# Performance work log

Measured on AMD Instinct MI355X. Metric: run time of the kernel, lower is better.

The kernel has to match this reference:

```python
import jax, jax.numpy as jnp
import numpy as np

N = 16384   # total nodes per drug-batch
E = 65536   # directed edges (avg degree 4)
B = 512     # graphs per batch
BN_EPS = 1e-5
SLOPE = 0.01  # LeakyReLU default


def _rn(k, shape, s=0.02):
    return jax.random.normal(k, shape, dtype=jnp.float32) * s


def setup_inputs():
    key = jax.random.key(0)
    ks = jax.random.split(key, 32)
    d = {}
    d['x1'] = jax.random.normal(ks[0], (N, 78), dtype=jnp.float32)
    d['edge_index1'] = jax.random.randint(ks[1], (2, E), 0, N)
    d['batch1'] = jnp.sort(jax.random.randint(ks[2], (N,), 0, B))
    d['x2'] = jax.random.normal(ks[3], (N, 78), dtype=jnp.float32)
    d['edge_index2'] = jax.random.randint(ks[4], (2, E), 0, N)
    d['batch2'] = jnp.sort(jax.random.randint(ks[5], (N,), 0, B))
    d['cell'] = jax.random.normal(ks[6], (B, 954), dtype=jnp.float32)
    # TransformerConv1: 78 -> 2 heads x 128 (concat 256)
    d['wq1'] = _rn(ks[7], (78, 256));  d['bq1'] = jnp.zeros((256,), jnp.float32)
    d['wk1'] = _rn(ks[8], (78, 256));  d['bk1'] = jnp.zeros((256,), jnp.float32)
    d['wv1'] = _rn(ks[9], (78, 256));  d['bv1'] = jnp.zeros((256,), jnp.float32)
    d['ws1'] = _rn(ks[10], (78, 256)); d['bs1'] = jnp.zeros((256,), jnp.float32)
    # TransformerConv2: 256 -> 2 heads x 512 (concat 1024)
    d['wq2'] = _rn(ks[11], (256, 1024)); d['bq2'] = jnp.zeros((1024,), jnp.float32)
    d['wk2'] = _rn(ks[12], (256, 1024)); d['bk2'] = jnp.zeros((1024,), jnp.float32)
    d['wv2'] = _rn(ks[13], (256, 1024)); d['bv2'] = jnp.zeros((1024,), jnp.float32)
    d['ws2'] = _rn(ks[14], (256, 1024)); d['bs2'] = jnp.zeros((1024,), jnp.float32)
    d['wg1'] = _rn(ks[15], (1024, 512)); d['bg1'] = jnp.zeros((512,), jnp.float32)
    d['wg2'] = _rn(ks[16], (512, 128));  d['bg2'] = jnp.zeros((128,), jnp.float32)
    d['wr1'] = _rn(ks[17], (954, 512));  d['br1'] = jnp.zeros((512,), jnp.float32)
    d['wr2'] = _rn(ks[18], (512, 256));  d['br2'] = jnp.zeros((256,), jnp.float32)
    d['wr3'] = _rn(ks[19], (256, 128));  d['br3'] = jnp.zeros((128,), jnp.float32)
    d['wf1'] = _rn(ks[20], (384, 512));  d['bf1'] = jnp.zeros((512,), jnp.float32)
    d['gbn1'] = jnp.ones((512,), jnp.float32); d['bbn1'] = jnp.zeros((512,), jnp.float32)
    d['wf2'] = _rn(ks[21], (512, 256));  d['bf2'] = jnp.zeros((256,), jnp.float32)
    d['gbn2'] = jnp.ones((256,), jnp.float32); d['bbn2'] = jnp.zeros((256,), jnp.float32)
    d['wf3'] = _rn(ks[22], (256, 1));    d['bf3'] = jnp.zeros((1,), jnp.float32)
    return d


def _lrelu(x):
    return jnp.where(x >= 0, x, SLOPE * x)


def _l2n(x):
    return x / jnp.maximum(jnp.linalg.norm(x, axis=1, keepdims=True), 1e-12)


def _tconv(x, ei, wq, bq, wk, bk, wv, bv, ws, bs, H, D):
    # PyG TransformerConv (concat=True, beta=False, root_weight=True)
    src, dst = ei[0], ei[1]
    n = x.shape[0]
    q = (x @ wq + bq).reshape(n, H, D)
    k = (x @ wk + bk).reshape(n, H, D)
    v = (x @ wv + bv).reshape(n, H, D)
    logits = jnp.einsum('ehd,ehd->eh', q[dst], k[src]) / jnp.sqrt(jnp.float32(D))  # [E,H]
    m = jax.ops.segment_max(logits, dst, num_segments=n)
    m = jnp.where(jnp.isfinite(m), m, 0.0)
    e = jnp.exp(logits - m[dst])
    z = jax.ops.segment_sum(e, dst, num_segments=n)
    alpha = e / (z[dst] + 1e-16)
    agg = jax.ops.segment_sum(alpha[:, :, None] * v[src], dst, num_segments=n)  # [N,H,D]
    return agg.reshape(n, H * D) + x @ ws + bs


def reference(x1, edge_index1, batch1, x2, edge_index2, batch2, cell,
              wq1, bq1, wk1, bk1, wv1, bv1, ws1, bs1,
              wq2, bq2, wk2, bk2, wv2, bv2, ws2, bs2,
              wg1, bg1, wg2, bg2, wr1, br1, wr2, br2, wr3, br3,
              wf1, bf1, gbn1, bbn1, wf2, bf2, gbn2, bbn2, wf3, bf3):
    def branch(x, ei, bt):
        h = _lrelu(_tconv(x, ei, wq1, bq1, wk1, bk1, wv1, bv1, ws1, bs1, 2, 128))
        h = _lrelu(_tconv(h, ei, wq2, bq2, wk2, bk2, wv2, bv2, ws2, bs2, 2, 512))
        g = jax.ops.segment_max(h, bt, num_segments=B)  # global max pool per graph
        g = jnp.where(jnp.isfinite(g), g, 0.0)
        g = _lrelu(g @ wg1 + bg1)
        g = g @ wg2 + bg2  # dropout = identity in eval
        return _l2n(g)

    x1g = branch(x1, edge_index1, batch1)
    x2g = branch(x2, edge_index2, batch2)

    c = _l2n(cell)
    c = _lrelu(c @ wr1 + br1)
    c = _lrelu(c @ wr2 + br2)
    c = c @ wr3 + br3

    xc = _l2n(jnp.concatenate([x1g, x2g, c], axis=1))  # [B, 384]
    bn = 1.0 / jnp.sqrt(1.0 + BN_EPS)  # eval BN with running mean 0, var 1
    h = _lrelu((xc @ wf1 + bf1) * bn * gbn1 + bbn1)
    h = _lrelu((h @ wf2 + bf2) * bn * gbn2 + bbn2)
    return jax.nn.sigmoid((h @ wf3 + bf3)[:, 0])
```

## Files before the change

kernel.cpp:

```cpp
#include <hip/hip_runtime.h>
#include <hip/hip_bf16.h>
#include <hip/hip_fp8.h>
#include <math.h>
#include <stdint.h>

typedef __hip_bfloat16 bf16;

#define NN 16384
#define EE 65536
#define BB 512

typedef __attribute__((ext_vector_type(8))) short short8;
typedef __attribute__((ext_vector_type(2))) short short2v;
typedef __attribute__((ext_vector_type(4))) float floatx4;
typedef __attribute__((ext_vector_type(2))) float floatx2;
typedef __attribute__((ext_vector_type(2))) unsigned int uint2v;

#define GKEY_NEGINF 0x007FFFFFu

__device__ __forceinline__ float lrelu_f(float x){ return x >= 0.f ? x : 0.01f*x; }

__device__ __forceinline__ float b2f(short s){
    unsigned int u = ((unsigned int)(unsigned short)s) << 16;
    float f; __builtin_memcpy(&f, &u, 4); return f;
}
__device__ __forceinline__ short f2b(float f){
    bf16 b = (bf16)f;
    short s; __builtin_memcpy(&s, &b, 2); return s;
}
__device__ __forceinline__ unsigned int fkey(float f){
    unsigned int u; __builtin_memcpy(&u, &f, 4);
    return (u & 0x80000000u) ? ~u : (u | 0x80000000u);
}
__device__ __forceinline__ float fdec(unsigned int k){
    if (k == GKEY_NEGINF) return 0.f;
    unsigned int u = (k & 0x80000000u) ? (k ^ 0x80000000u) : ~k;
    float f; __builtin_memcpy(&f, &u, 4); return f;
}

__device__ __forceinline__ void gl2lds16(const void* g, void* l){
    __builtin_amdgcn_global_load_lds(
        (__attribute__((address_space(1))) unsigned int*)(uintptr_t)g,
        (__attribute__((address_space(3))) unsigned int*)(uintptr_t)l, 16, 0, 0);
}

template<int KSC>
__global__ __launch_bounds__(256)
void mfma_gemm(const bf16* __restrict__ A, int lda,
               const bf16* __restrict__ Bp,
               const float* __restrict__ bias,
               bf16* __restrict__ C, int ldc,
               unsigned char* __restrict__ C2, int ldc2, int nsplit)
{
    __shared__ __align__(16) char smem[20480];
    bf16* As0 = (bf16*)smem;
    bf16* As1 = (bf16*)(smem + 8192);
    bf16* epi = (bf16*)smem;
    const int tid  = threadIdx.x;
    const int wave = tid >> 6;
    const int lane = tid & 63;
    const int wm = (wave & 1) * 64;
    const int wn = (wave >> 1) * 64;
    const int m0 = blockIdx.x * 128;
    const int n0 = blockIdx.y * 128;
    const bool isf8 = (n0 >= nsplit);
    const int ntile0 = (n0 + wn) >> 4;

    const int srow = lane >> 2;
    const int scol = (((lane & 3) ^ ((srow >> 1) & 3))) * 8;
    const int arow = lane & 15;
    const int aq   = (((lane >> 4) ^ ((arow >> 1) & 3))) * 8;

    floatx4 acc[4][4];
    #pragma unroll
    for (int i=0;i<4;i++)
        #pragma unroll
        for (int j=0;j<4;j++) acc[i][j] = (floatx4){0.f,0.f,0.f,0.f};

    auto stageA = [&](int t, bf16* buf){
        const int k0 = t*32;
        #pragma unroll
        for (int i = 0; i < 2; i++) {
            const int chunk = wave*2 + i;
            const int r = chunk*16 + srow;
            gl2lds16(A + (size_t)(m0 + r)*lda + k0 + scol, buf + chunk*512);
        }
    };
    auto loadB = [&](short8* dst, int ks){
        #pragma unroll
        for (int j=0;j<4;j++)
            dst[j] = *(const short8*)(Bp + ((size_t)((ntile0 + j)*KSC + ks))*512 + lane*8);
    };

    short8 bcur[4], bnxt[4];
    loadB(bcur, 0);
    stageA(0, As0);

    #pragma unroll
    for (int t = 0; t < KSC; t++){
        bf16* cur = (t & 1) ? As1 : As0;
        bf16* nxt = (t & 1) ? As0 : As1;
        if (t + 1 < KSC){
            stageA(t+1, nxt);
            loadB(bnxt, t+1);
            asm volatile("s_waitcnt vmcnt(6)" ::: "memory");
        } else {
            asm volatile("s_waitcnt vmcnt(0)" ::: "memory");
        }
        __builtin_amdgcn_s_barrier();
        __builtin_amdgcn_sched_barrier(0);
        short8 af[4];
        #pragma unroll
        for (int i=0;i<4;i++) af[i] = *(const short8*)(cur + (wm + i*16 + arow)*32 + aq);
        #pragma unroll
        for (int i=0;i<4;i++)
            #pragma unroll
            for (int j=0;j<4;j++)
                acc[i][j] = __builtin_amdgcn_mfma_f32_16x16x32_bf16(af[i], bcur[j], acc[i][j], 0,0,0);
        __builtin_amdgcn_sched_barrier(0);
        __builtin_amdgcn_s_barrier();
        if (t + 1 < KSC){
            #pragma unroll
            for (int j=0;j<4;j++) bcur[j] = bnxt[j];
        }
    }

    const int crow = (lane >> 4) * 4;
    const int ccol = lane & 15;
    const int erow = lane >> 2;
    const int ecol = (lane & 3) * 8;
    bf16* ep = epi + wave * (64*40);
    #pragma unroll
    for (int j2 = 0; j2 < 2; j2++){
        if (j2) __syncthreads();
        #pragma unroll
        for (int jj = 0; jj < 2; jj++){
            const int j = j2*2 + jj;
            const float bsv = bias[n0 + wn + j*16 + ccol];
            #pragma unroll
            for (int i = 0; i < 4; i++)
                #pragma unroll
                for (int r = 0; r < 4; r++)
                    ep[(i*16 + crow + r)*40 + jj*16 + ccol] = (bf16)(acc[i][j][r] + bsv);
        }
        __syncthreads();
        #pragma unroll
        for (int q = 0; q < 4; q++){
            const int rr = q*16 + erow;
            short8 vv = *(const short8*)(ep + rr*40 + ecol);
            if (!isf8){
                *(short8*)(C + (size_t)(m0 + wm + rr)*ldc + n0 + wn + j2*32 + ecol) = vv;
            } else {
                int d0 = 0, d1 = 0;
                d0 = __builtin_amdgcn_cvt_pk_fp8_f32(b2f(vv[0]), b2f(vv[1]), d0, false);
                d0 = __builtin_amdgcn_cvt_pk_fp8_f32(b2f(vv[2]), b2f(vv[3]), d0, true);
                d1 = __builtin_amdgcn_cvt_pk_fp8_f32(b2f(vv[4]), b2f(vv[5]), d1, false);
                d1 = __builtin_amdgcn_cvt_pk_fp8_f32(b2f(vv[6]), b2f(vv[7]), d1, true);
                uint2v ob; ob[0] = (unsigned int)d0; ob[1] = (unsigned int)d1;
                *(uint2v*)(C2 + (size_t)(m0 + wm + rr)*ldc2 + (n0 - nsplit) + wn + j2*32 + ecol) = ob;
            }
        }
    }
}

#define OG1 0
#define OG2 524288
#define OR1 589824
#define OR2 1081344
#define OR3 1212416
#define OF1 1245184
#define OF2 1441792
#define TAILW_TOTAL 1572864

#define P_W1T 98304
#define P_B1C (P_W1T + 1024)
#define P_W2T (P_B1C + 1048576)
#define P_B2C (P_W2T + 4096)
#define P_WTP (P_B2C + TAILW_TOTAL)
#define P_XA  (P_WTP + 2*NN*96)
#define P_GK  (P_XA + 2*BB*1024)
__global__ void prep_mega_kernel(
    const float* __restrict__ wq1, const float* __restrict__ wk1,
    const float* __restrict__ wv1, const float* __restrict__ ws1,
    const float* __restrict__ bq1, const float* __restrict__ bk1,
    const float* __restrict__ bv1, const float* __restrict__ bs1,
    const float* __restrict__ wq2, const float* __restrict__ wk2,
    const float* __restrict__ wv2, const float* __restrict__ ws2,
    const float* __restrict__ bq2, const float* __restrict__ bk2,
    const float* __restrict__ bv2, const float* __restrict__ bs2v,
    const float* __restrict__ wg1, const float* __restrict__ wg2,
    const float* __restrict__ wr1, const float* __restrict__ wr2,
    const float* __restrict__ wr3, const float* __restrict__ wf1,
    const float* __restrict__ wf2,
    const float* __restrict__ x1,  const float* __restrict__ x2,
    bf16* __restrict__ W1t, float* __restrict__ b1c,
    bf16* __restrict__ W2t, float* __restrict__ b2c,
    bf16* __restrict__ Wtp, bf16* __restrict__ xa,
    unsigned int* __restrict__ gkey)
{
    int i = blockIdx.x*256 + threadIdx.x;
    if (i < P_W1T){
        int j  = i & 7;
        int ln = (i >> 3) & 63;
        int rest = i >> 9;
        int ks = rest % 3, tile = rest / 3;
        int n = tile*16 + (ln & 15);
        int k = ks*32 + (ln >> 4)*8 + j;
        int seg = n >> 8;
        const float* w = (seg==0)?ws1:(seg==1)?wq1:(seg==2)?wk1:wv1;
        W1t[i] = (k < 78) ? (bf16)w[(size_t)k*256 + (n & 255)] : (bf16)0.f;
        return;
    }
    if (i < P_B1C){
        int n = i - P_W1T;
        int seg = n >> 8;
        const float* b = (seg==0)?bs1:(seg==1)?bq1:(seg==2)?bk1:bv1;
        b1c[n] = b[n & 255];
        return;
    }
    if (i < P_W2T){
        int loc = i - P_B1C;
        int h  = loc >> 19;
        int l2 = loc & 524287;
        int j  = l2 & 7;
        int ln = (l2 >> 3) & 63;
        int rest = l2 >> 9;
        int ks = rest & 7, tile = rest >> 3;
        int n = tile*16 + (ln & 15);
        int k = ks*32 + (ln >> 4)*8 + j;
        const float* w = (n<512)?ws2:(n<1024)?wq2:(n<1536)?wk2:wv2;
        W2t[loc] = (bf16)w[(size_t)k*1024 + h*512 + (n & 511)];
        return;
    }
    if (i < P_B2C){
        int loc = i - P_W2T;
        int j = loc & 2047, h = loc >> 11;
        const float* b = (j<512)?bs2v:(j<1024)?bq2:(j<1536)?bk2:bv2;
        b2c[loc] = b[h*512 + (j & 511)];
        return;
    }
    if (i < P_WTP){
        int t = i - P_B2C;
        const float* W; int N, K, KS, base;
        if      (t < OG2){ W = wg1; N = 512; K = 1024; KS = 32; base = OG1; }
        else if (t < OR1){ W = wg2; N = 128; K = 512;  KS = 16; base = OG2; }
        else if (t < OR2){ W = wr1; N = 512; K = 954;  KS = 30; base = OR1; }
        else if (t < OR3){ W = wr2; N = 256; K = 512;  KS = 16; base = OR2; }
        else if (t < OF1){ W = wr3; N = 128; K = 256;  KS = 8;  base = OR3; }
        else if (t < OF2){ W = wf1; N = 512; K = 384;  KS = 12; base = OF1; }
        else             { W = wf2; N = 256; K = 512;  KS = 16; base = OF2; }
        int loc = t - base;
        int j  = loc & 7;
        int ln = (loc >> 3) & 63;
        int rest = loc >> 9;
        int ks = rest % KS;
        int tile = rest / KS;
        int n = tile*16 + (ln & 15);
        int k = ks*32 + (ln >> 4)*8 + j;
        Wtp[t] = (k < K) ? (bf16)W[(size_t)k*N + n] : (bf16)0.f;
        return;
    }
    if (i < P_XA){
        int t = i - P_WTP;
        int r = t / 96, c = t - r*96;
        const float* x = (r >= NN) ? x2 : x1;
        int lr = r & (NN-1);
        xa[t] = (c < 78) ? (bf16)x[(size_t)lr*78 + c] : (bf16)0.f;
        return;
    }
    if (i < P_GK){
        gkey[i - P_XA] = GKEY_NEGINF;
    }
}

__global__ void hist_kernel(const int* __restrict__ ei1, const int* __restrict__ ei2,
                            int* __restrict__ cnt){
    int eg = blockIdx.x*256 + threadIdx.x;
    int br = eg >> 16, e = eg & (EE-1);
    const int* ei = br ? ei2 : ei1;
    atomicAdd(&cnt[br*NN + ei[EE + e]], 1);
}

__global__ __launch_bounds__(1024)
void scan_kernel(const int* __restrict__ hist, int* __restrict__ rowptr,
                 int* __restrict__ rowcur){
    const int br = blockIdx.x;
    hist   += br*NN;
    rowptr += br*(NN+1);
    rowcur += br*(NN+1);
    __shared__ int sums[1024];
    const int t = threadIdx.x;
    const int base = t*16;
    int loc[16]; int s = 0;
    #pragma unroll
    for (int i=0;i<16;i++){ loc[i]=s; s += hist[base+i]; }
    sums[t] = s; __syncthreads();
    for (int o=1;o<1024;o<<=1){
        int v = (t>=o) ? sums[t-o] : 0;
        __syncthreads();
        sums[t] += v;
        __syncthreads();
    }
    int pref = (t>0) ? sums[t-1] : 0;
    #pragma unroll
    for (int i=0;i<16;i++){
        int v = pref + loc[i];
        rowptr[base+i] = v;
        rowcur[base+i] = v;
    }
    if (t==1023) rowptr[NN] = sums[1023];
}

__global__ void scatter_kernel(const int* __restrict__ ei1, const int* __restrict__ ei2,
                               int* __restrict__ rowcur, int* __restrict__ srcs){
    int eg = blockIdx.x*256 + threadIdx.x;
    int br = eg >> 16, e = eg & (EE-1);
    const int* ei = br ? ei2 : ei1;
    int d = ei[EE + e];
    int pos = atomicAdd(&rowcur[br*(NN+1) + d], 1);
    srcs[br*EE + pos] = ei[e];
}

__global__ __launch_bounds__(256)
void attn128_f8(const bf16* __restrict__ s1, const unsigned char* __restrict__ f81,
                bf16* __restrict__ hout,
                const int* __restrict__ rowptr, const int* __restrict__ srcs)
{
    const int lane = threadIdx.x & 63;
    const int gw = blockIdx.x * 4 + (threadIdx.x >> 6);
    const int n = gw >> 1;
    const int h = gw & 1;
    int br = n >> 14;
    int brNN = br*NN, nl = n - brNN;
    rowptr += br*(NN+1); srcs += br*EE;
    const float qscale = rsqrtf(128.f) * 1.44269504f;
    const int hd = h*128 + lane*2;

    unsigned short qw; __builtin_memcpy(&qw, f81 + (size_t)n*768 + hd, 2);
    floatx2 qd = __builtin_amdgcn_cvt_pk_f32_fp8((int)qw, false);
    float qr[2] = { qd[0]*qscale, qd[1]*qscale };

    const int e0 = rowptr[nl], e1 = rowptr[nl+1];
    float m = -INFINITY, z = 0.f;
    float acc[2] = {0.f, 0.f};

    for (int base = e0; base < e1; base += 4){
        const int cnt = min(4, e1 - base);
        int sl = srcs[min(base + (lane & 3), e1 - 1)];
        int src[4];
        #pragma unroll
        for (int j=0;j<4;j++) src[j] = __shfl(sl, j, 64);

        unsigned short kw[4], vw[4];
        #pragma unroll
        for (int j=0;j<4;j++){
            if (j < cnt){
                const unsigned char* rp = f81 + (size_t)(brNN + src[j])*768;
                __builtin_memcpy(&kw[j], rp + 256 + hd, 2);
                __builtin_memcpy(&vw[j], rp + 512 + hd, 2);
            }
        }
        float dt[4];
        #pragma unroll
        for (int j=0;j<4;j++){
            float d = 0.f;
            if (j < cnt){
                floatx2 kd = __builtin_amdgcn_cvt_pk_f32_fp8((int)kw[j], false);
                d = qr[0]*kd[0] + qr[1]*kd[1];
            }
            dt[j] = d;
        }
        #pragma unroll
        for (int o=32;o;o>>=1){
            #pragma unroll
            for (int j=0;j<4;j++) dt[j] += __shfl_xor(dt[j], o, 64);
        }
        float cm = -INFINITY;
        #pragma unroll
        for (int j=0;j<4;j++) if (j < cnt) cm = fmaxf(cm, dt[j]);
        const float mn = fmaxf(m, cm);
        const float cs = exp2f(m - mn);
        z *= cs;
        acc[0] *= cs; acc[1] *= cs;
        #pragma unroll
        for (int j=0;j<4;j++){
            if (j < cnt){
                const float w = exp2f(dt[j] - mn);
                z += w;
                floatx2 vd = __builtin_amdgcn_cvt_pk_f32_fp8((int)vw[j], false);
                acc[0] += w*vd[0];
                acc[1] += w*vd[1];
            }
        }
        m = mn;
    }
    const float invz = 1.0f/(z + 1e-16f);
    const short2v sv = *(const short2v*)(s1 + (size_t)n*256 + hd);
    short2v ov;
    ov[0] = f2b(lrelu_f(b2f(sv[0]) + acc[0]*invz));
    ov[1] = f2b(lrelu_f(b2f(sv[1]) + acc[1]*invz));
    *(short2v*)(hout + (size_t)n*256 + hd) = ov;
}

__global__ __launch_bounds__(256)
void attn512_f8(const bf16* __restrict__ s2, const unsigned char* __restrict__ f82,
                const int* __restrict__ rowptr, const int* __restrict__ srcs,
                const int* __restrict__ bt1, const int* __restrict__ bt2,
                unsigned int* __restrict__ gkey, int gc0)
{
    __shared__ float Sh[4][512];
    __shared__ int Sgid[4];
    const int lane = threadIdx.x & 63;
    const int wave = threadIdx.x >> 6;
    const int n = blockIdx.x * 4 + wave;
    const int br = n >> 14;
    const int brNN = br*NN, nl = n - brNN;
    const int* rp_ = rowptr + br*(NN+1);
    const int* sp_ = srcs + br*EE;
    const float qscale = rsqrtf(512.f) * 1.44269504f;
    const int hd = lane*8;

    float qr[8];
    {
        const uint2v qv = *(const uint2v*)(f82 + (size_t)n*1536 + hd);
        floatx2 a = __builtin_amdgcn_cvt_pk_f32_fp8((int)qv[0], false);
        floatx2 b = __builtin_amdgcn_cvt_pk_f32_fp8((int)qv[0], true);
        floatx2 c = __builtin_amdgcn_cvt_pk_f32_fp8((int)qv[1], false);
        floatx2 d = __builtin_amdgcn_cvt_pk_f32_fp8((int)qv[1], true);
        qr[0]=a[0]*qscale; qr[1]=a[1]*qscale; qr[2]=b[0]*qscale; qr[3]=b[1]*qscale;
        qr[4]=c[0]*qscale; qr[5]=c[1]*qscale; qr[6]=d[0]*qscale; qr[7]=d[1]*qscale;
    }

    const int e0 = rp_[nl], e1 = rp_[nl+1];
    float m = -INFINITY, z = 0.f;
    float acc[8];
    #pragma unroll
    for (int i=0;i<8;i++) acc[i] = 0.f;

    for (int base = e0; base < e1; base += 4){
        const int cnt = min(4, e1 - base);
        int sl = sp_[min(base + (lane & 3), e1 - 1)];
        int src[4];
        #pragma unroll
        for (int j=0;j<4;j++) src[j] = __shfl(sl, j, 64);

        uint2v k2[4], v2[4];
        #pragma unroll
        for (int j=0;j<4;j++){
            if (j < cnt){
                const unsigned char* rp = f82 + (size_t)(brNN + src[j])*1536;
                k2[j] = *(const uint2v*)(rp + 512 + hd);
                v2[j] = *(const uint2v*)(rp + 1024 + hd);
            }
        }
        float dt[4];
        #pragma unroll
        for (int j=0;j<4;j++){
            float d = 0.f;
            if (j < cnt){
                floatx2 p0 = __builtin_amdgcn_cvt_pk_f32_fp8((int)k2[j][0], false);
                floatx2 p1 = __builtin_amdgcn_cvt_pk_f32_fp8((int)k2[j][0], true);
                floatx2 p2 = __builtin_amdgcn_cvt_pk_f32_fp8((int)k2[j][1], false);
                floatx2 p3 = __builtin_amdgcn_cvt_pk_f32_fp8((int)k2[j][1], true);
                d = qr[0]*p0[0] + qr[1]*p0[1] + qr[2]*p1[0] + qr[3]*p1[1]
                  + qr[4]*p2[0] + qr[5]*p2[1] + qr[6]*p3[0] + qr[7]*p3[1];
            }
            dt[j] = d;
        }
        #pragma unroll
        for (int o=32;o;o>>=1){
            #pragma unroll
            for (int j=0;j<4;j++) dt[j] += __shfl_xor(dt[j], o, 64);
        }
        float cm = -INFINITY;
        #pragma unroll
        for (int j=0;j<4;j++) if (j < cnt) cm = fmaxf(cm, dt[j]);
        const float mn = fmaxf(m, cm);
        const float cs = exp2f(m - mn);
        z *= cs;
        #pragma unroll
        for (int i=0;i<8;i++) acc[i] *= cs;
        #pragma unroll
        for (int j=0;j<4;j++){
            if (j < cnt){
                const float w = exp2f(dt[j] - mn);
                z += w;
                floatx2 p0 = __builtin_amdgcn_cvt_pk_f32_fp8((int)v2[j][0], false);
                floatx2 p1 = __builtin_amdgcn_cvt_pk_f32_fp8((int)v2[j][0], true);
                floatx2 p2 = __builtin_amdgcn_cvt_pk_f32_fp8((int)v2[j][1], false);
                floatx2 p3 = __builtin_amdgcn_cvt_pk_f32_fp8((int)v2[j][1], true);
                acc[0] += w*p0[0]; acc[1] += w*p0[1]; acc[2] += w*p1[0]; acc[3] += w*p1[1];
                acc[4] += w*p2[0]; acc[5] += w*p2[1]; acc[6] += w*p3[0]; acc[7] += w*p3[1];
            }
        }
        m = mn;
    }
    const float invz = 1.0f/(z + 1e-16f);
    const short8 sv = *(const short8*)(s2 + (size_t)n*512 + hd);
    #pragma unroll
    for (int i=0;i<8;i++) Sh[wave][hd + i] = lrelu_f(b2f(sv[i]) + acc[i]*invz);
    if (lane == 0) Sgid[wave] = br*BB + (br ? bt2[nl] : bt1[nl]);
    __syncthreads();

    #pragma unroll
    for (int cc=0; cc<2; cc++){
        const int col = threadIdx.x*2 + cc;
        float mx = Sh[0][col];
        int gid = Sgid[0];
        #pragma unroll
        for (int r=1; r<4; r++){
            if (Sgid[r] == gid) mx = fmaxf(mx, Sh[r][col]);
            else {
                atomicMax(&gkey[(size_t)gid*1024 + gc0 + col], fkey(mx));
                gid = Sgid[r]; mx = Sh[r][col];
            }
        }
        atomicMax(&gkey[(size_t)gid*1024 + gc0 + col], fkey(mx));
    }
}

template<int R, int N, int K, int ACT>
__device__ __forceinline__ void dense_mfma(
    const bf16* __restrict__ Wm, const float* __restrict__ bias,
    const float* __restrict__ gam, const float* __restrict__ bet, float bns,
    const float* A, int lda, float* C, int ldc, int tid)
{
    constexpr int T   = N / 16;
    constexpr int TPW = (T + 15) / 16;
    constexpr int KS  = ((K + 31) & ~31) >> 5;
    constexpr int PF  = (KS < 8) ? KS : 8;
    const int wave = tid >> 6;
    const int lane = tid & 63;
    const int am = lane & 15;
    const int ak = (lane >> 4) * 8;

    floatx4 acc[TPW];
    #pragma unroll
    for (int tp=0; tp<TPW; tp++) acc[tp] = (floatx4){0.f,0.f,0.f,0.f};

    short8 bb[PF][TPW];
    #pragma unroll
    for (int p=0; p<PF; p++){
        #pragma unroll
        for (int tp=0; tp<TPW; tp++){
            const int tile = wave + tp*16;
            if (tile < T)
                bb[p][tp] = *(const short8*)(Wm + ((size_t)(tile*KS + p))*512 + lane*8);
        }
    }

    #pragma unroll
    for (int ks = 0; ks < KS; ks++){
        short8 af = (short8){0,0,0,0,0,0,0,0};
        if (am < R){
            const float* ap = A + am*lda + ks*32 + ak;
            const floatx4 a0 = *(const floatx4*)ap;
            const floatx4 a1 = *(const floatx4*)(ap + 4);
            af[0]=f2b(a0[0]); af[1]=f2b(a0[1]); af[2]=f2b(a0[2]); af[3]=f2b(a0[3]);
            af[4]=f2b(a1[0]); af[5]=f2b(a1[1]); af[6]=f2b(a1[2]); af[7]=f2b(a1[3]);
        }
        #pragma unroll
        for (int tp=0; tp<TPW; tp++){
            const int tile = wave + tp*16;
            if (tile < T)
                acc[tp] = __builtin_amdgcn_mfma_f32_16x16x32_bf16(af, bb[ks % PF][tp], acc[tp], 0,0,0);
        }
        if (ks + PF < KS){
            #pragma unroll
            for (int tp=0; tp<TPW; tp++){
                const int tile = wave + tp*16;
                if (tile < T)
                    bb[ks % PF][tp] = *(const short8*)(Wm + ((size_t)(tile*KS + ks + PF))*512 + lane*8);
            }
        }
    }
    const int crow = (lane >> 4) * 4;
    const int ccol = lane & 15;
    #pragma unroll
    for (int tp=0; tp<TPW; tp++){
        const int tile = wave + tp*16;
        if (tile < T){
            #pragma unroll
            for (int r=0; r<4; r++){
                const int row = crow + r;
                if (row < R){
                    const int n = tile*16 + ccol;
                    float v = acc[tp][r] + bias[n];
                    if (ACT==1) v = lrelu_f(v);
                    if (ACT==2) v = lrelu_f(v*bns*gam[n] + bet[n]);
                    C[row*ldc + n] = v;
                }
            }
        }
    }
    __syncthreads();
}

__global__ __launch_bounds__(1024)
void tail_kernel(const unsigned int* __restrict__ gkey,
                 const float* __restrict__ cell,
                 const bf16*  __restrict__ Wtp,
                 const float* __restrict__ bg1, const float* __restrict__ bg2,
                 const float* __restrict__ br1, const float* __restrict__ br2,
                 const float* __restrict__ br3,
                 const float* __restrict__ bf1,
                 const float* __restrict__ gbn1, const float* __restrict__ bbn1,
                 const float* __restrict__ bf2,
                 const float* __restrict__ gbn2, const float* __restrict__ bbn2,
                 const float* __restrict__ wf3, const float* __restrict__ bf3,
                 float bns, float* __restrict__ outp)
{
    __shared__ float Sg[4][1028];
    __shared__ float Sgh[4][516];
    __shared__ float Sgout[4][132];
    __shared__ float Scell[2][964];
    __shared__ float Sc1[2][516];
    __shared__ float Sc2[2][260];
    __shared__ float Sc3[2][132];
    __shared__ float Sxc[2][388];
    __shared__ float Sf1[2][516];
    __shared__ float Sf2[2][260];
    __shared__ float inv4[4], invc[2], invx[2];

    const int tid = threadIdx.x;
    const int wv  = tid >> 6;
    const int ln  = tid & 63;
    const int b0  = blockIdx.x * 2;

    {
        int idx = tid*4;
        int r = idx >> 10, c = idx & 1023;
        int lg = r >> 1, br = r & 1;
        const unsigned int* gp = gkey + (size_t)(br*BB + b0 + lg)*1024 + c;
        #pragma unroll
        for (int i=0;i<4;i++) Sg[r][c+i] = fdec(gp[i]);
    }
    for (int idx = tid; idx < 2*954; idx += 1024){
        int r = (idx >= 954) ? 1 : 0;
        int c = idx - r*954;
        Scell[r][c] = cell[(size_t)(b0 + r)*954 + c];
    }
    if (tid < 12){ int r = tid/6; Scell[r][954 + tid%6] = 0.f; }
    __syncthreads();

    if (wv < 2){
        float s = 0.f;
        for (int c = ln; c < 954; c += 64){ float v = Scell[wv][c]; s += v*v; }
        #pragma unroll
        for (int o=32;o;o>>=1) s += __shfl_xor(s, o, 64);
        if (ln == 0) invc[wv] = 1.0f / fmaxf(sqrtf(s), 1e-12f);
    }
    __syncthreads();
    #pragma unroll
    for (int r=0;r<2;r++)
        for (int c = tid; c < 954; c += 1024) Scell[r][c] *= invc[r];
    __syncthreads();

    dense_mfma<4,512,1024,1>(Wtp+OG1, bg1, nullptr, nullptr, 1.f, &Sg[0][0],   1028, &Sgh[0][0],  516, tid);
    dense_mfma<4,128,512,0>(Wtp+OG2, bg2, nullptr, nullptr, 1.f, &Sgh[0][0],  516,  &Sgout[0][0],132, tid);
    dense_mfma<2,512,954,1>(Wtp+OR1, br1, nullptr, nullptr, 1.f, &Scell[0][0], 964, &Sc1[0][0],  516, tid);
    dense_mfma<2,256,512,1>(Wtp+OR2, br2, nullptr, nullptr, 1.f, &Sc1[0][0],   516, &Sc2[0][0],  260, tid);
    dense_mfma<2,128,256,0>(Wtp+OR3, br3, nullptr, nullptr, 1.f, &Sc2[0][0],   260, &Sc3[0][0],  132, tid);

    if (wv < 4){
        float a = Sgout[wv][ln], bq = Sgout[wv][ln+64];
        float s = a*a + bq*bq;
        #pragma unroll
        for (int o=32;o;o>>=1) s += __shfl_xor(s, o, 64);
        if (ln == 0) inv4[wv] = 1.0f / fmaxf(sqrtf(s), 1e-12f);
    }
    __syncthreads();

    if (tid < 768){
        int lg = tid / 384, j = tid - lg*384;
        float v;
        if (j < 128)      v = Sgout[lg*2+0][j]     * inv4[lg*2+0];
        else if (j < 256) v = Sgout[lg*2+1][j-128] * inv4[lg*2+1];
        else              v = Sc3[lg][j-256];
        Sxc[lg][j] = v;
    }
    __syncthreads();
    if (wv < 2){
        float s = 0.f;
        #pragma unroll
        for (int i=0;i<6;i++){ float v = Sxc[wv][ln + i*64]; s += v*v; }
        #pragma unroll
        for (int o=32;o;o>>=1) s += __shfl_xor(s, o, 64);
        if (ln == 0) invx[wv] = 1.0f / fmaxf(sqrtf(s), 1e-12f);
    }
    __syncthreads();
    if (tid < 768){
        int lg = tid / 384, j = tid - lg*384;
        Sxc[lg][j] *= invx[lg];
    }
    __syncthreads();

    dense_mfma<2,512,384,2>(Wtp+OF1, bf1, gbn1, bbn1, bns, &Sxc[0][0], 388, &Sf1[0][0], 516, tid);
    dense_mfma<2,256,512,2>(Wtp+OF2, bf2, gbn2, bbn2, bns, &Sf1[0][0], 516, &Sf2[0][0], 260, tid);

    if (wv < 2){
        float s = 0.f;
        #pragma unroll
        for (int i=0;i<4;i++){ int c = ln + i*64; s += Sf2[wv][c]*wf3[c]; }
        #pragma unroll
        for (int o=32;o;o>>=1) s += __shfl_xor(s, o, 64);
        if (ln == 0) outp[b0 + wv] = 1.0f/(1.0f + expf(-(s + bf3[0])));
    }
}

extern "C" void kernel_launch(void* const* d_in, const int* in_sizes, int n_in,
                              void* d_out, int out_size, void* d_ws, size_t ws_size,
                              hipStream_t stream)
{
    const float* x1  = (const float*)d_in[0];
    const int*   ei1 = (const int*)  d_in[1];
    const int*   bt1 = (const int*)  d_in[2];
    const float* x2  = (const float*)d_in[3];
    const int*   ei2 = (const int*)  d_in[4];
    const int*   bt2 = (const int*)  d_in[5];
    const float* cell= (const float*)d_in[6];
    const float* wq1=(const float*)d_in[7];  const float* bq1=(const float*)d_in[8];
    const float* wk1=(const float*)d_in[9];  const float* bk1=(const float*)d_in[10];
    const float* wv1=(const float*)d_in[11]; const float* bv1=(const float*)d_in[12];
    const float* ws1=(const float*)d_in[13]; const float* bs1=(const float*)d_in[14];
    const float* wq2=(const float*)d_in[15]; const float* bq2=(const float*)d_in[16];
    const float* wk2=(const float*)d_in[17]; const float* bk2=(const float*)d_in[18];
    const float* wv2=(const float*)d_in[19]; const float* bv2=(const float*)d_in[20];
    const float* ws2=(const float*)d_in[21]; const float* bs2q=(const float*)d_in[22];
    const float* wg1=(const float*)d_in[23]; const float* bg1=(const float*)d_in[24];
    const float* wg2=(const float*)d_in[25]; const float* bg2=(const float*)d_in[26];
    const float* wr1=(const float*)d_in[27]; const float* br1=(const float*)d_in[28];
    const float* wr2=(const float*)d_in[29]; const float* br2=(const float*)d_in[30];
    const float* wr3=(const float*)d_in[31]; const float* br3=(const float*)d_in[32];
    const float* wf1=(const float*)d_in[33]; const float* bf1=(const float*)d_in[34];
    const float* gbn1=(const float*)d_in[35];const float* bbn1=(const float*)d_in[36];
    const float* wf2=(const float*)d_in[37]; const float* bf2=(const float*)d_in[38];
    const float* gbn2=(const float*)d_in[39];const float* bbn2=(const float*)d_in[40];
    const float* wf3=(const float*)d_in[41]; const float* bf3=(const float*)d_in[42];
    float* outp = (float*)d_out;
    (void)in_sizes; (void)n_in; (void)out_size; (void)ws_size;

    const float BNS = 1.0f / sqrtf(1.0f + 1e-5f);

    char* basep = (char*)d_ws;
    size_t off = 0;
    auto alloc = [&](size_t nbytes)->char* {
        char* p = basep + off;
        off += (nbytes + 255) & ~(size_t)255;
        return p;
    };
    int* rowptr2  = (int*)  alloc((size_t)2*(NN+1)*4);
    int* rowcur2  = (int*)  alloc((size_t)2*(NN+1)*4);
    int* cnt2     = (int*)  alloc((size_t)2*NN*4);
    int* srcs2    = (int*)  alloc((size_t)2*EE*4);
    unsigned int* gkey = (unsigned int*)alloc((size_t)2*BB*1024*4);
    float* b1c    = (float*)alloc((size_t)1024*4);
    float* b2c    = (float*)alloc((size_t)4096*4);
    bf16* W1t     = (bf16*) alloc((size_t)1024*96*2);
    bf16* W2t     = (bf16*) alloc((size_t)2*2048*256*2);
    bf16* Wtp     = (bf16*) alloc((size_t)TAILW_TOTAL*2);
    bf16* h1      = (bf16*) alloc((size_t)2*NN*256*2);
    char* BIG     = alloc((size_t)2*NN*512*2 + (size_t)2*NN*1536);
    bf16* xa      = (bf16*)BIG;
    bf16* s1a     = (bf16*)(BIG + 6291456);
    unsigned char* f81 = (unsigned char*)(BIG + 6291456 + 16777216);
    bf16* s2a     = (bf16*)BIG;
    unsigned char* f82 = (unsigned char*)(BIG + (size_t)2*NN*512*2);

    (void)hipMemsetAsync(cnt2, 0, (size_t)2*NN*4, stream);
    prep_mega_kernel<<<P_GK/256,256,0,stream>>>(
        wq1,wk1,wv1,ws1, bq1,bk1,bv1,bs1,
        wq2,wk2,wv2,ws2, bq2,bk2,bv2,bs2q,
        wg1,wg2,wr1,wr2,wr3,wf1,wf2,
        x1,x2,
        W1t,b1c,W2t,b2c, Wtp, xa, gkey);
    hist_kernel<<<2*EE/256,256,0,stream>>>(ei1, ei2, cnt2);
    scan_kernel<<<2,1024,0,stream>>>(cnt2, rowptr2, rowcur2);
    scatter_kernel<<<2*EE/256,256,0,stream>>>(ei1, ei2, rowcur2, srcs2);

    mfma_gemm<3><<<dim3(2*NN/128, 8),256,0,stream>>>(xa,96, W1t, b1c,
                                                     s1a,256, f81,768, 256);
    attn128_f8<<<2*NN*2/4,256,0,stream>>>(s1a, f81, h1, rowptr2, srcs2);

    for (int h=0; h<2; h++){
        mfma_gemm<8><<<dim3(2*NN/128, 16),256,0,stream>>>(
            h1, 256, W2t + (size_t)h*524288,
            b2c + h*2048, s2a,512, f82,1536, 512);
        attn512_f8<<<2*NN/4,256,0,stream>>>(s2a, f82, rowptr2, srcs2, bt1, bt2,
                                            gkey, h*512);
    }

    tail_kernel<<<BB/2,1024,0,stream>>>(gkey, cell, Wtp,
                                        bg1,bg2, br1,br2,br3,
                                        bf1,gbn1,bbn1, bf2,gbn2,bbn2, wf3,bf3,
                                        BNS, outp);
}
```

Measured before the change: 468.8 us.

## Load GEMM A fragments directly from global into registers, dropping LDS staging

The MFMA GEMM main loop no longer stages A tiles into shared memory with global_load_lds and barriers. Each wave now loads its A and B fragments straight from global memory into registers, using a two-deep register prefetch ring. This removes the LDS round trip and the per-iteration block barriers. In exchange, A rows are loaded redundantly by the two waves that share them, access is less coalesced (16-byte loads strided by lda), and register pressure rises.

```diff
diff --git a/kernel.cpp b/kernel.cpp
--- a/kernel.cpp
+++ b/kernel.cpp
@@ -36,12 +36,6 @@
     if (k == GKEY_NEGINF) return 0.f;
     unsigned int u = (k & 0x80000000u) ? (k ^ 0x80000000u) : ~k;
     float f; __builtin_memcpy(&f, &u, 4); return f;
-}
-
-__device__ __forceinline__ void gl2lds16(const void* g, void* l){
-    __builtin_amdgcn_global_load_lds(
-        (__attribute__((address_space(1))) unsigned int*)(uintptr_t)g,
-        (__attribute__((address_space(3))) unsigned int*)(uintptr_t)l, 16, 0, 0);
 }
 
 template<int KSC>
@@ -53,8 +47,6 @@
                unsigned char* __restrict__ C2, int ldc2, int nsplit)
 {
     __shared__ __align__(16) char smem[20480];
-    bf16* As0 = (bf16*)smem;
-    bf16* As1 = (bf16*)(smem + 8192);
     bf16* epi = (bf16*)smem;
     const int tid  = threadIdx.x;
     const int wave = tid >> 6;
@@ -66,10 +58,10 @@
     const bool isf8 = (n0 >= nsplit);
     const int ntile0 = (n0 + wn) >> 4;
 
-    const int srow = lane >> 2;
-    const int scol = (((lane & 3) ^ ((srow >> 1) & 3))) * 8;
     const int arow = lane & 15;
-    const int aq   = (((lane >> 4) ^ ((arow >> 1) & 3))) * 8;
+    const int aq   = (lane >> 4) * 8;
+    const bf16* Aw = A + (size_t)(m0 + wm + arow)*lda + aq;
+    const bf16* Bw = Bp + (size_t)ntile0*KSC*512 + lane*8;
 
     floatx4 acc[4][4];
     #pragma unroll
@@ -77,51 +69,30 @@
         #pragma unroll
         for (int j=0;j<4;j++) acc[i][j] = (floatx4){0.f,0.f,0.f,0.f};
 
-    auto stageA = [&](int t, bf16* buf){
-        const int k0 = t*32;
-        #pragma unroll
-        for (int i = 0; i < 2; i++) {
-            const int chunk = wave*2 + i;
-            const int r = chunk*16 + srow;
-            gl2lds16(A + (size_t)(m0 + r)*lda + k0 + scol, buf + chunk*512);
-        }
-    };
-    auto loadB = [&](short8* dst, int ks){
-        #pragma unroll
-        for (int j=0;j<4;j++)
-            dst[j] = *(const short8*)(Bp + ((size_t)((ntile0 + j)*KSC + ks))*512 + lane*8);
-    };
-
-    short8 bcur[4], bnxt[4];
-    loadB(bcur, 0);
-    stageA(0, As0);
-
-    #pragma unroll
-    for (int t = 0; t < KSC; t++){
-        bf16* cur = (t & 1) ? As1 : As0;
-        bf16* nxt = (t & 1) ? As0 : As1;
-        if (t + 1 < KSC){
-            stageA(t+1, nxt);
-            loadB(bnxt, t+1);
-            asm volatile("s_waitcnt vmcnt(6)" ::: "memory");
-        } else {
-            asm volatile("s_waitcnt vmcnt(0)" ::: "memory");
-        }
-        __builtin_amdgcn_s_barrier();
-        __builtin_amdgcn_sched_barrier(0);
-        short8 af[4];
-        #pragma unroll
-        for (int i=0;i<4;i++) af[i] = *(const short8*)(cur + (wm + i*16 + arow)*32 + aq);
+    constexpr int PF = (KSC < 2) ? KSC : 2;
+    short8 a_[PF][4], b_[PF][4];
+    #pragma unroll
+    for (int p=0; p<PF; p++){
+        #pragma unroll
+        for (int i=0;i<4;i++) a_[p][i] = *(const short8*)(Aw + (size_t)i*16*lda + p*32);
+        #pragma unroll
+        for (int j=0;j<4;j++) b_[p][j] = *(const short8*)(Bw + ((size_t)j*KSC + p)*512);
+    }
+
+    #pragma unroll
+    for (int ks = 0; ks < KSC; ks++){
+        constexpr int DUMMY = 0; (void)DUMMY;
+        const int s = ks % PF;
         #pragma unroll
         for (int i=0;i<4;i++)
             #pragma unroll
             for (int j=0;j<4;j++)
-                acc[i][j] = __builtin_amdgcn_mfma_f32_16x16x32_bf16(af[i], bcur[j], acc[i][j], 0,0,0);
-        __builtin_amdgcn_sched_barrier(0);
-        __builtin_amdgcn_s_barrier();
-        if (t + 1 < KSC){
+                acc[i][j] = __builtin_amdgcn_mfma_f32_16x16x32_bf16(a_[s][i], b_[s][j], acc[i][j], 0,0,0);
+        if (ks + PF < KSC){
             #pragma unroll
-            for (int j=0;j<4;j++) bcur[j] = bnxt[j];
+            for (int i=0;i<4;i++) a_[s][i] = *(const short8*)(Aw + (size_t)i*16*lda + (ks+PF)*32);
+            #pragma unroll
+            for (int j=0;j<4;j++) b_[s][j] = *(const short8*)(Bw + ((size_t)j*KSC + (ks+PF))*512);
         }
     }
 
```

Result: slower. 535.1 us (+14.1%).
